# Kernel tuning notes

Measured on AMD Instinct MI355X. Metric: run time of the kernel, lower is better.

The kernel has to match this reference:

```python
import jax, jax.numpy as jnp
import numpy as np

B, A, N_IN, N_POINTS = 64, 256, 512, 2048


def _sq_cdist(u, v):
    # |u_i - v_j|^2 via expansion, abs() as in the torch original
    d = -2.0 * (u @ v.T) + (u * u).sum(1)[:, None] + (v * v).sum(1)[None, :]
    return jnp.abs(d)


def setup_inputs() -> dict:
    key = jax.random.key(0)
    k1, k2, k3, k4 = jax.random.split(key, 4)
    x = jax.random.normal(k1, (B, A, N_IN), dtype=jnp.float32)
    atom_mask = jax.random.bernoulli(k2, 0.8, (B, A))  # ragged valid-atom mask
    inducing_points = jax.random.normal(k3, (N_POINTS, N_IN), dtype=jnp.float32)
    gamma = (1.0 + 0.25 * jax.random.normal(k4, (N_IN,), dtype=jnp.float32)) * np.sqrt(N_IN).astype(np.float32)
    return {"x": x, "atom_mask": atom_mask, "inducing_points": inducing_points, "gamma": gamma}


def reference(x, atom_mask, inducing_points, gamma):
    b, a, n_in = x.shape
    m = atom_mask.astype(x.dtype)                      # [B, A]
    mf = m[..., None]                                  # [B, A, 1]
    n = m.sum()
    # masked mean / unbiased std over valid atoms (torch .std is ddof=1)
    mean = (x * mf).sum((0, 1)) / n                    # [n_in]
    var = (((x - mean) ** 2) * mf).sum((0, 1)) / (n - 1.0)
    std = jnp.sqrt(var) + 1e-5                         # [n_in]
    xn = (x - mean) / std * mf                         # zero out padded atoms

    g2 = gamma ** 2 + 0.001                            # [n_in]
    z = (xn / g2).reshape(b * a, n_in)                 # [N, n_in]
    zi = inducing_points / g2                          # [M, n_in]

    Kx = jnp.exp(-_sq_cdist(z, zi))                    # [N, M]
    Kind = jnp.exp(-_sq_cdist(zi, zi))                 # [M, M]
    Kinv = jnp.linalg.inv(Kind + 0.05 * jnp.eye(Kind.shape[0], dtype=x.dtype))

    t = Kx @ Kinv                                      # [N, M]
    x_new = ((t @ inducing_points) * std + mean).reshape(b, a, n_in) * mf
    var_out = (1.0 - (t * Kx).sum(-1)).reshape(b, a) * m
    return x_new, var_out
```

## Files before the change

### kernel.cpp

```cpp
#include <hip/hip_runtime.h>
#include <math.h>
#include <stdint.h>

namespace {

constexpr int NROW = 16384;
constexpr int NF   = 512;
constexpr int MIND = 2048;
constexpr float CC = 0.98f;

typedef _Float16 half8 __attribute__((ext_vector_type(8)));
typedef float floatx4 __attribute__((ext_vector_type(4)));

__device__ __forceinline__ void gload16(const void* g, void* l) {
  __builtin_amdgcn_global_load_lds(
      (__attribute__((address_space(1))) void*)g,
      (__attribute__((address_space(3))) void*)l, 16, 0, 0);
}

#define MEMFENCE asm volatile("" ::: "memory")
#define GATE(N) asm volatile("s_waitcnt vmcnt(" #N ")" ::: "memory")

__global__ __launch_bounds__(256) void stats_kernel(
    const float* __restrict__ x, const int* __restrict__ mask,
    float* __restrict__ sum, float* __restrict__ sumsq, float* __restrict__ cnt)
{
  const int t = threadIdx.x;
  const int row0 = blockIdx.x * 64;
  float s0 = 0.f, s1 = 0.f, q0 = 0.f, q1 = 0.f, c = 0.f;
  for (int r = 0; r < 64; ++r) {
    const int row = row0 + r;
    const float m = (mask[row] != 0) ? 1.f : 0.f;
    const float v0 = x[(size_t)row * NF + t];
    const float v1 = x[(size_t)row * NF + t + 256];
    s0 += m * v0; q0 += m * v0 * v0;
    s1 += m * v1; q1 += m * v1 * v1;
    c += m;
  }
  atomicAdd(&sum[t], s0);        atomicAdd(&sum[t + 256], s1);
  atomicAdd(&sumsq[t], q0);      atomicAdd(&sumsq[t + 256], q1);
  if (t == 0) atomicAdd(cnt, c);
}

__global__ __launch_bounds__(256) void finalize_stats(
    const float* __restrict__ sum, const float* __restrict__ sumsq,
    const float* __restrict__ cnt, const float* __restrict__ gamma,
    float* __restrict__ meanv, float* __restrict__ stdv,
    float* __restrict__ zsv, float* __restrict__ giv)
{
  const int f = blockIdx.x * 256 + threadIdx.x;
  const float n = cnt[0];
  const float mu = sum[f] / n;
  const float var = (sumsq[f] - sum[f] * mu) / (n - 1.0f);
  const float sd = sqrtf(var) + 1e-5f;
  const float g = gamma[f];
  const float g2 = g * g + 0.001f;
  meanv[f] = mu;
  stdv[f]  = sd;
  zsv[f]   = 1.0f / (sd * g2);
  giv[f]   = 1.0f / g2;
}

__global__ __launch_bounds__(256) void make_z(
    const float* __restrict__ x, const int* __restrict__ mask,
    const float* __restrict__ ip, const float* __restrict__ meanv,
    const float* __restrict__ zsv, const float* __restrict__ giv,
    _Float16* __restrict__ Zh, _Float16* __restrict__ Zih,
    float* __restrict__ rnorm, float* __restrict__ cnorm)
{
  const int row = blockIdx.x;
  const int t = threadIdx.x;
  float v0, v1;
  if (row < NROW) {
    const float m = (mask[row] != 0) ? 1.f : 0.f;
    v0 = (x[(size_t)row * NF + t      ] - meanv[t      ]) * zsv[t      ] * m;
    v1 = (x[(size_t)row * NF + t + 256] - meanv[t + 256]) * zsv[t + 256] * m;
    const _Float16 h0 = (_Float16)v0, h1 = (_Float16)v1;
    Zh[(size_t)row * NF + t] = h0;
    Zh[(size_t)row * NF + t + 256] = h1;
    v0 = (float)h0; v1 = (float)h1;
  } else {
    const int r = row - NROW;
    v0 = ip[(size_t)r * NF + t      ] * giv[t      ];
    v1 = ip[(size_t)r * NF + t + 256] * giv[t + 256];
    const _Float16 h0 = (_Float16)v0, h1 = (_Float16)v1;
    Zih[(size_t)r * NF + t] = h0;
    Zih[(size_t)r * NF + t + 256] = h1;
    v0 = (float)h0; v1 = (float)h1;
  }
  float nrm = v0 * v0 + v1 * v1;
  #pragma unroll
  for (int off = 32; off; off >>= 1) nrm += __shfl_xor(nrm, off);
  __shared__ float red[4];
  if ((t & 63) == 0) red[t >> 6] = nrm;
  __syncthreads();
  if (t == 0) {
    const float s = red[0] + red[1] + red[2] + red[3];
    if (row < NROW) rnorm[row] = s; else cnorm[row - NROW] = s;
  }
}

template <int EPI>
__global__ __launch_bounds__(512, 2) void mfma_gemm256(
    const _Float16* __restrict__ A, const _Float16* __restrict__ B,
    int M, int N, int K,
    const float* __restrict__ rn, const float* __restrict__ cn,
    _Float16* __restrict__ DKout,
    const _Float16* __restrict__ DK, const float* __restrict__ u,
    float* __restrict__ varacc)
{
  __shared__ __align__(16) _Float16 Asmem[4][256 * 32];
  __shared__ __align__(16) _Float16 Bsmem[4][256 * 32];

  const int tid = threadIdx.x;
  const int w = tid >> 6, L = tid & 63;
  const int wm = w >> 2, wn = w & 3;
  const int lq = L >> 4, lr = L & 15;
  const int bn = blockIdx.x, bm = blockIdx.y;
  const int NT = K >> 5;

  const int srow  = tid >> 2;
  const int sslot = tid & 3;
  const int gslot = sslot ^ ((tid >> 3) & 3);
  const _Float16* Ag = A + (size_t)(bm * 256 + srow) * K + gslot * 8;
  const _Float16* Bg = B + (size_t)(bn * 256 + srow) * K + gslot * 8;
  const size_t rstride = (size_t)128 * K;
  const int ldst = srow * 32 + sslot * 8;

  const int fswz = (lq ^ ((lr >> 1) & 3)) * 8;
  const int aoff = (wm * 128 + lr) * 32 + fswz;
  const int boff = (wn * 64  + lr) * 32 + fswz;

  floatx4 acc[8][4] = {};

  auto stageA = [&](int t) {
    _Float16* dst = Asmem[t & 3] + ldst;
    const _Float16* src = Ag + (size_t)t * 32;
    gload16(src, dst);
    gload16(src + rstride, dst + 128 * 32);
  };
  auto stageB = [&](int t) {
    _Float16* dst = Bsmem[t & 3] + ldst;
    const _Float16* src = Bg + (size_t)t * 32;
    gload16(src, dst);
    gload16(src + rstride, dst + 128 * 32);
  };

  stageA(0); stageB(0);
  if (NT > 1) { stageA(1); stageB(1); }
  if (NT > 2) { stageA(2); stageB(2); }
  if (NT > 2)      { GATE(8); }
  else if (NT > 1) { GATE(4); }
  else             { GATE(0); }
  __builtin_amdgcn_s_barrier();
  MEMFENCE;

  for (int t = 0; t < NT; ++t) {
    const _Float16* As = Asmem[t & 3];
    const _Float16* Bs = Bsmem[t & 3];
    half8 af[4], bf[4], af2[4];

    #pragma unroll
    for (int mi = 0; mi < 4; ++mi) af[mi] = *(const half8*)&As[aoff + mi * 512];
    #pragma unroll
    for (int ni = 0; ni < 4; ++ni) bf[ni] = *(const half8*)&Bs[boff + ni * 512];
    if (t + 3 < NT) stageA(t + 3);
    MEMFENCE;
    __builtin_amdgcn_s_barrier();
    MEMFENCE;
    __builtin_amdgcn_s_setprio(1);
    #pragma unroll
    for (int mi = 0; mi < 4; ++mi)
      #pragma unroll
      for (int ni = 0; ni < 4; ++ni)
        acc[mi][ni] = __builtin_amdgcn_mfma_f32_16x16x32_f16(
            af[mi], bf[ni], acc[mi][ni], 0, 0, 0);
    __builtin_amdgcn_s_setprio(0);

    #pragma unroll
    for (int mi = 0; mi < 4; ++mi)
      af2[mi] = *(const half8*)&As[aoff + (mi + 4) * 512];
    if (t + 3 < NT) stageB(t + 3);
    if (t + 4 <= NT)      { GATE(8); }
    else if (t + 3 == NT) { GATE(4); }
    else if (t + 2 == NT) { GATE(0); }
    __builtin_amdgcn_s_barrier();
    MEMFENCE;
    __builtin_amdgcn_s_setprio(1);
    #pragma unroll
    for (int mi = 0; mi < 4; ++mi)
      #pragma unroll
      for (int ni = 0; ni < 4; ++ni)
        acc[mi + 4][ni] = __builtin_amdgcn_mfma_f32_16x16x32_f16(
            af2[mi], bf[ni], acc[mi + 4][ni], 0, 0, 0);
    __builtin_amdgcn_s_setprio(0);
  }

  const int grb = bm * 256 + wm * 128;
  const int gcb = bn * 256 + wn * 64;

  if constexpr (EPI == 0) {
    #pragma unroll
    for (int mi = 0; mi < 8; ++mi)
      #pragma unroll
      for (int e = 0; e < 4; ++e) {
        const int gr = grb + mi * 16 + lq * 4 + e;
        const float rni = rn[gr];
        #pragma unroll
        for (int ni = 0; ni < 4; ++ni) {
          const int gc = gcb + ni * 16 + lr;
          const float d = rni + cn[gc] - 2.f * acc[mi][ni][e];
          DKout[(size_t)gr * N + gc] = (_Float16)(expf(-fabsf(d)) - CC);
        }
      }
  } else {
    #pragma unroll
    for (int mi = 0; mi < 8; ++mi)
      #pragma unroll
      for (int e = 0; e < 4; ++e) {
        const int gr = grb + mi * 16 + lq * 4 + e;
        float partial = 0.f;
        #pragma unroll
        for (int ni = 0; ni < 4; ++ni) {
          const int gc = gcb + ni * 16 + lr;
          const float tv = acc[mi][ni][e] + CC * u[gc];
          partial += tv * (CC + (float)DK[(size_t)gr * N + gc]);
        }
        partial += __shfl_xor(partial, 1);
        partial += __shfl_xor(partial, 2);
        partial += __shfl_xor(partial, 4);
        partial += __shfl_xor(partial, 8);
        if (lr == 0) atomicAdd(&varacc[gr], partial);
      }
  }
}

template <int EPI>
__global__ __launch_bounds__(256) void mfma_gemm(
    const _Float16* __restrict__ A, const _Float16* __restrict__ B,
    int M, int N, int K,
    const float* __restrict__ rn, const float* __restrict__ cn,
    _Float16* __restrict__ DKout, float* __restrict__ Cf,
    const _Float16* __restrict__ DK, const float* __restrict__ u,
    float* __restrict__ varacc,
    const float* __restrict__ colsumR,
    const float* __restrict__ stdv, const float* __restrict__ meanv,
    const int* __restrict__ mask)
{
  __shared__ __align__(16) _Float16 As[128 * 32];
  __shared__ __align__(16) _Float16 Bs[128 * 32];
  const int tid = threadIdx.x;
  const int w = tid >> 6, L = tid & 63;
  const int wm = w >> 1, wn = w & 1;
  const int bn = blockIdx.x, bm = blockIdx.y;
  const int lq = L >> 4;
  const int lr = L & 15;

  floatx4 acc[4][4] = {};

  const _Float16* Ag = A + (size_t)(bm * 128) * K;
  const _Float16* Bg = B + (size_t)(bn * 128) * K;
  const int srow = w * 32 + (L >> 2);
  const int scol = (L & 3) * 8;

  for (int k0 = 0; k0 < K; k0 += 32) {
    #pragma unroll
    for (int t = 0; t < 2; ++t) {
      const int r = srow + t * 16;
      gload16(Ag + (size_t)r * K + k0 + scol, As + r * 32 + scol);
      gload16(Bg + (size_t)r * K + k0 + scol, Bs + r * 32 + scol);
    }
    __syncthreads();
    half8 af[4], bf[4];
    #pragma unroll
    for (int mi = 0; mi < 4; ++mi)
      af[mi] = *(const half8*)&As[(wm * 64 + mi * 16 + lr) * 32 + lq * 8];
    #pragma unroll
    for (int ni = 0; ni < 4; ++ni)
      bf[ni] = *(const half8*)&Bs[(wn * 64 + ni * 16 + lr) * 32 + lq * 8];
    #pragma unroll
    for (int mi = 0; mi < 4; ++mi)
      #pragma unroll
      for (int ni = 0; ni < 4; ++ni)
        acc[mi][ni] = __builtin_amdgcn_mfma_f32_16x16x32_f16(
            af[mi], bf[ni], acc[mi][ni], 0, 0, 0);
    __syncthreads();
  }

  const int grb = bm * 128 + wm * 64;
  const int gcb = bn * 128 + wn * 64;

  if constexpr (EPI == 3) {
    #pragma unroll
    for (int mi = 0; mi < 4; ++mi)
      #pragma unroll
      for (int e = 0; e < 4; ++e) {
        const int gr = grb + mi * 16 + lq * 4 + e;
        const float mrow = (mask[gr] != 0) ? 1.f : 0.f;
        #pragma unroll
        for (int ni = 0; ni < 4; ++ni) {
          const int gc = gcb + ni * 16 + lr;
          const float v = acc[mi][ni][e] + CC * colsumR[gc];
          Cf[(size_t)gr * N + gc] = (v * stdv[gc] + meanv[gc]) * mrow;
        }
      }
  } else {
    #pragma unroll
    for (int mi = 0; mi < 4; ++mi)
      #pragma unroll
      for (int e = 0; e < 4; ++e) {
        const int gr = grb + mi * 16 + lq * 4 + e;
        const float rni = rn[gr];
        #pragma unroll
        for (int ni = 0; ni < 4; ++ni) {
          const int gc = gcb + ni * 16 + lr;
          const float d = rni + cn[gc] - 2.f * acc[mi][ni][e];
          float kx = expf(-fabsf(d));
          if (gr == gc) kx += 0.05f;
          Cf[(size_t)gr * N + gc] = kx;
        }
      }
  }
}

__global__ __launch_bounds__(256) void gemm_f32(
    const float* __restrict__ A, const float* __restrict__ B,
    float* __restrict__ C, int M, int N, int K)
{
  constexpr int BM = 64, BN = 64, BK = 16;
  const int tid = threadIdx.x;
  const int tx = tid % 16, ty = tid / 16;
  const int bn = blockIdx.x, bm = blockIdx.y;
  __shared__ float As[BK][BM + 4];
  __shared__ float Bs[BK][BN + 4];
  float acc[4][4] = {};
  const float* Ag = A + (size_t)bm * BM * K;
  const float* Bg = B + bn * BN;
  for (int k0 = 0; k0 < K; k0 += BK) {
    {
      const int r = tid >> 2, c4 = (tid & 3) << 2;
      const float4 av = *(const float4*)(Ag + (size_t)r * K + k0 + c4);
      As[c4 + 0][r] = av.x; As[c4 + 1][r] = av.y;
      As[c4 + 2][r] = av.z; As[c4 + 3][r] = av.w;
      const int kr = tid / 16, nc = (tid % 16) << 2;
      *(float4*)&Bs[kr][nc] = *(const float4*)(Bg + (size_t)(k0 + kr) * N + nc);
    }
    __syncthreads();
    #pragma unroll
    for (int kk = 0; kk < BK; ++kk) {
      const float4 a4 = *(const float4*)&As[kk][ty * 4];
      const float4 b4 = *(const float4*)&Bs[kk][tx * 4];
      const float a[4] = {a4.x, a4.y, a4.z, a4.w};
      const float b[4] = {b4.x, b4.y, b4.z, b4.w};
      #pragma unroll
      for (int i = 0; i < 4; ++i)
        #pragma unroll
        for (int j = 0; j < 4; ++j) acc[i][j] += a[i] * b[j];
    }
    __syncthreads();
  }
  #pragma unroll
  for (int i = 0; i < 4; ++i) {
    float4 o4; o4.x = acc[i][0]; o4.y = acc[i][1]; o4.z = acc[i][2]; o4.w = acc[i][3];
    *(float4*)(C + (size_t)(bm * BM + ty * 4 + i) * N + bn * BN + tx * 4) = o4;
  }
}


__global__ __launch_bounds__(256) void gj_diag(
    float* __restrict__ A, float* __restrict__ Pall, int k)
{
  const int o = k * 64;
  __shared__ float D[64][68];
  const int t = threadIdx.x;
  #pragma unroll
  for (int l = 0; l < 4; ++l) {
    const int v = t + l * 256;
    const int r = v >> 4, c4 = (v & 15) << 2;
    *(float4*)&D[r][c4] = *(const float4*)(A + (size_t)(o + r) * MIND + o + c4);
  }
  __syncthreads();
  const int i = t >> 2, c0 = (t & 3) * 16;
  for (int s = 0; s < 64; ++s) {
    const float p = 1.0f / D[s][s];
    if (t < 64 && t != s) D[s][t] *= p;
    __syncthreads();
    if (i != s) {
      const float f = D[i][s];
      #pragma unroll
      for (int c = c0; c < c0 + 16; c += 4) {
        float4 ds = *(const float4*)&D[s][c];
        float4 di = *(const float4*)&D[i][c];
        di.x -= f * ds.x; di.y -= f * ds.y; di.z -= f * ds.z; di.w -= f * ds.w;
        *(float4*)&D[i][c] = di;
      }
      if (s >= c0 && s < c0 + 16) D[i][s] = -f * p;
    }
    if (t == 0) D[s][s] = p;
    __syncthreads();
  }
  float* P = Pall + k * 4096;
  #pragma unroll
  for (int l = 0; l < 4; ++l) {
    const int v = t + l * 256;
    const int r = v >> 4, c4 = (v & 15) << 2;
    const float4 dv = *(const float4*)&D[r][c4];
    *(float4*)(P + r * 64 + c4) = dv;
    *(float4*)(A + (size_t)(o + r) * MIND + o + c4) = dv;
  }
}

__global__ __launch_bounds__(256) void gj_prep(
    const float* __restrict__ A, const float* __restrict__ Pall,
    float* __restrict__ CP, float* __restrict__ Bsave, int k)
{
  const int o = k * 64;
  const int t = threadIdx.x;
  if (blockIdx.x >= 32) {
    const int j0 = (blockIdx.x - 32) * 64;
    #pragma unroll
    for (int l = 0; l < 4; ++l) {
      const int v = t + l * 256;
      const int r = v >> 4, c4 = (v & 15) << 2;
      *(float4*)(Bsave + r * MIND + j0 + c4) =
          *(const float4*)(A + (size_t)(o + r) * MIND + j0 + c4);
    }
    return;
  }
  const int i0 = blockIdx.x * 64;
  if (i0 == o) return;
  const float* P = Pall + k * 4096;
  __shared__ float At[64][68];
  __shared__ float Pl[64][68];
  #pragma unroll
  for (int l = 0; l < 4; ++l) {
    const int v = t + l * 256;
    const int r = v >> 4, c4 = (v & 15) << 2;
    const float4 av = *(const float4*)(A + (size_t)(i0 + r) * MIND + o + c4);
    At[c4 + 0][r] = av.x; At[c4 + 1][r] = av.y;
    At[c4 + 2][r] = av.z; At[c4 + 3][r] = av.w;
    *(float4*)&Pl[r][c4] = *(const float4*)(P + r * 64 + c4);
  }
  __syncthreads();
  const int ty = t >> 4, tx = t & 15;
  float acc[4][4] = {};
  for (int s = 0; s < 64; ++s) {
    const float4 a4 = *(const float4*)&At[s][ty * 4];
    const float4 b4 = *(const float4*)&Pl[s][tx * 4];
    const float a[4] = {a4.x, a4.y, a4.z, a4.w};
    const float b[4] = {b4.x, b4.y, b4.z, b4.w};
    #pragma unroll
    for (int i = 0; i < 4; ++i)
      #pragma unroll
      for (int j = 0; j < 4; ++j) acc[i][j] += a[i] * b[j];
  }
  #pragma unroll
  for (int i = 0; i < 4; ++i) {
    float4 o4; o4.x = acc[i][0]; o4.y = acc[i][1]; o4.z = acc[i][2]; o4.w = acc[i][3];
    *(float4*)(CP + (i0 + ty * 4 + i) * 64 + tx * 4) = o4;
  }
}

__global__ __launch_bounds__(256) void gj_apply(
    float* __restrict__ A, float* __restrict__ Pall,
    const float* __restrict__ CP, const float* __restrict__ Bsave, int k)
{
  const int o = k * 64;
  const int i0 = blockIdx.y * 64, j0 = blockIdx.x * 64;
  const int t = threadIdx.x;

  if (i0 == o && j0 == o) return;

  if (j0 == o) {
    #pragma unroll
    for (int l = 0; l < 4; ++l) {
      const int v = t + l * 256;
      const int r = v >> 4, c4 = (v & 15) << 2;
      float4 x = *(const float4*)(CP + (i0 + r) * 64 + c4);
      x.x = -x.x; x.y = -x.y; x.z = -x.z; x.w = -x.w;
      *(float4*)(A + (size_t)(i0 + r) * MIND + o + c4) = x;
    }
    return;
  }

  __shared__ float S1[64 * 68];
  __shared__ float S2[64 * 68];
  #define DD(r, c) S1[(r) * 68 + (c)]

  const bool isrow = (i0 == o);
  const float* Lsrc = isrow ? (Pall + k * 4096) : (CP + i0 * 64);
  #pragma unroll
  for (int l = 0; l < 4; ++l) {
    const int v = t + l * 256;
    const int r = v >> 4, c4 = (v & 15) << 2;
    const float4 lv = *(const float4*)(Lsrc + r * 64 + c4);
    S1[(c4 + 0) * 68 + r] = lv.x; S1[(c4 + 1) * 68 + r] = lv.y;
    S1[(c4 + 2) * 68 + r] = lv.z; S1[(c4 + 3) * 68 + r] = lv.w;
    *(float4*)&S2[r * 68 + c4] = *(const float4*)(Bsave + r * MIND + j0 + c4);
  }
  __syncthreads();
  const int ty = t >> 4, tx = t & 15;
  float acc[4][4] = {};
  for (int s = 0; s < 64; ++s) {
    const float4 a4 = *(const float4*)&S1[s * 68 + ty * 4];
    const float4 b4 = *(const float4*)&S2[s * 68 + tx * 4];
    const float a[4] = {a4.x, a4.y, a4.z, a4.w};
    const float b[4] = {b4.x, b4.y, b4.z, b4.w};
    #pragma unroll
    for (int i = 0; i < 4; ++i)
      #pragma unroll
      for (int j = 0; j < 4; ++j) acc[i][j] += a[i] * b[j];
  }

  if (isrow) {
    #pragma unroll
    for (int i = 0; i < 4; ++i) {
      float4 o4; o4.x = acc[i][0]; o4.y = acc[i][1]; o4.z = acc[i][2]; o4.w = acc[i][3];
      *(float4*)(A + (size_t)(o + ty * 4 + i) * MIND + j0 + tx * 4) = o4;
    }
    return;
  }

  const bool isdiagnext = (i0 == o + 64) && (j0 == o + 64);
  if (!isdiagnext) {
    #pragma unroll
    for (int i = 0; i < 4; ++i) {
      float* cp = A + (size_t)(i0 + ty * 4 + i) * MIND + j0 + tx * 4;
      float4 cv = *(const float4*)cp;
      cv.x -= acc[i][0]; cv.y -= acc[i][1]; cv.z -= acc[i][2]; cv.w -= acc[i][3];
      *(float4*)cp = cv;
    }
    return;
  }

  __syncthreads();
  #pragma unroll
  for (int i = 0; i < 4; ++i) {
    const float4 cv = *(const float4*)(A + (size_t)(i0 + ty * 4 + i) * MIND + j0 + tx * 4);
    DD(ty * 4 + i, tx * 4 + 0) = cv.x - acc[i][0];
    DD(ty * 4 + i, tx * 4 + 1) = cv.y - acc[i][1];
    DD(ty * 4 + i, tx * 4 + 2) = cv.z - acc[i][2];
    DD(ty * 4 + i, tx * 4 + 3) = cv.w - acc[i][3];
  }
  __syncthreads();
  const int di = t >> 2, c0 = (t & 3) * 16;
  for (int s = 0; s < 64; ++s) {
    const float p = 1.0f / DD(s, s);
    if (t < 64 && t != s) DD(s, t) *= p;
    __syncthreads();
    if (di != s) {
      const float f = DD(di, s);
      #pragma unroll
      for (int c = c0; c < c0 + 16; c += 4) {
        float4 ds = *(const float4*)&DD(s, c);
        float4 dv = *(const float4*)&DD(di, c);
        dv.x -= f * ds.x; dv.y -= f * ds.y; dv.z -= f * ds.z; dv.w -= f * ds.w;
        *(float4*)&DD(di, c) = dv;
      }
      if (s >= c0 && s < c0 + 16) DD(di, s) = -f * p;
    }
    if (t == 0) DD(s, s) = p;
    __syncthreads();
  }
  float* Pn = Pall + (k + 1) * 4096;
  #pragma unroll
  for (int l = 0; l < 4; ++l) {
    const int v = t + l * 256;
    const int r = v >> 4, c4 = (v & 15) << 2;
    const float4 dv = *(const float4*)&DD(r, c4);
    *(float4*)(Pn + r * 64 + c4) = dv;
    *(float4*)(A + (size_t)(i0 + r) * MIND + j0 + c4) = dv;
  }
  #undef DD
}

__global__ __launch_bounds__(256) void rowsum_kernel(
    const float* __restrict__ Ai, float* __restrict__ u)
{
  const int row = blockIdx.x * 4 + (threadIdx.x >> 6);
  const int lane = threadIdx.x & 63;
  float s = 0.f;
  for (int c = lane; c < MIND; c += 64) s += Ai[(size_t)row * MIND + c];
  #pragma unroll
  for (int off = 32; off; off >>= 1) s += __shfl_xor(s, off);
  if (lane == 0) u[row] = s;
}

typedef _Float16 half4v __attribute__((ext_vector_type(4)));
__global__ __launch_bounds__(256) void cast_half4(
    const float* __restrict__ s, _Float16* __restrict__ d)
{
  const int i = (blockIdx.x * 256 + threadIdx.x) * 4;
  const float4 v = *(const float4*)(s + i);
  half4v h; h.x = (_Float16)v.x; h.y = (_Float16)v.y;
  h.z = (_Float16)v.z; h.w = (_Float16)v.w;
  *(half4v*)(d + i) = h;
}

__global__ __launch_bounds__(256) void transpose_cast(
    const float* __restrict__ R, _Float16* __restrict__ Rt)
{
  __shared__ float T[64][65];
  const int j0 = blockIdx.x * 64;
  const int f0 = blockIdx.y * 64;
  const int t = threadIdx.x;
  #pragma unroll
  for (int l = 0; l < 16; ++l) {
    const int idx = t + l * 256;
    T[idx >> 6][idx & 63] = R[(size_t)(j0 + (idx >> 6)) * NF + f0 + (idx & 63)];
  }
  __syncthreads();
  #pragma unroll
  for (int l = 0; l < 16; ++l) {
    const int idx = t + l * 256;
    const int fr = idx >> 6, jc = idx & 63;
    Rt[(size_t)(f0 + fr) * MIND + j0 + jc] = (_Float16)T[jc][fr];
  }
}

__global__ __launch_bounds__(256) void colsum_kernel(
    const float* __restrict__ R, float* __restrict__ cs)
{
  const int b = blockIdx.x;
  const int t = threadIdx.x;
  float s0 = 0.f, s1 = 0.f;
  for (int r = 0; r < 64; ++r) {
    s0 += R[(size_t)(b * 64 + r) * NF + t];
    s1 += R[(size_t)(b * 64 + r) * NF + t + 256];
  }
  atomicAdd(&cs[t], s0); atomicAdd(&cs[t + 256], s1);
}

__global__ __launch_bounds__(256) void var_finalize(
    const float* __restrict__ varacc, const int* __restrict__ mask,
    float* __restrict__ outv)
{
  const int i = blockIdx.x * 256 + threadIdx.x;
  const float m = (mask[i] != 0) ? 1.f : 0.f;
  outv[i] = (1.0f - varacc[i]) * m;
}

}

extern "C" void kernel_launch(void* const* d_in, const int* in_sizes, int n_in,
                              void* d_out, int out_size, void* d_ws, size_t ws_size,
                              hipStream_t stream)
{
  (void)in_sizes; (void)n_in; (void)out_size; (void)ws_size;
  const float* x     = (const float*)d_in[0];
  const int*   mask  = (const int*)d_in[1];
  const float* ip    = (const float*)d_in[2];
  const float* gamma = (const float*)d_in[3];
  float* out = (float*)d_out;

  float* w       = (float*)d_ws;
  float* sum     = w;
  float* sumsq   = w + 512;
  float* cnt     = w + 1024;
  float* varacc  = w + 1536;
  float* colsumR = w + 17920;
  float* meanv   = w + 18432;
  float* stdv    = w + 18944;
  float* zsv     = w + 19456;
  float* giv     = w + 19968;
  float* rnorm   = w + 20480;
  float* cnorm   = w + 36864;
  float* u       = w + 38912;
  float* Ai      = w + 40960;
  float* R       = w + 4235264;
  float* Pall    = w + 5283840;
  float* CP      = w + 5414912;
  float* Bsave   = w + 5545984;
  _Float16* hb   = (_Float16*)(w + 5677056);
  _Float16* Zh   = hb;
  _Float16* Zih  = hb + 8388608;
  _Float16* DK   = hb + 9437184;
  _Float16* Kih  = hb + 42991616;
  _Float16* Rt   = hb + 47185920;

  hipMemsetAsync(w, 0, 18432 * sizeof(float), stream);

  stats_kernel<<<256, 256, 0, stream>>>(x, mask, sum, sumsq, cnt);
  finalize_stats<<<2, 256, 0, stream>>>(sum, sumsq, cnt, gamma, meanv, stdv, zsv, giv);
  make_z<<<NROW + MIND, 256, 0, stream>>>(x, mask, ip, meanv, zsv, giv, Zh, Zih, rnorm, cnorm);

  mfma_gemm256<0><<<dim3(MIND / 256, NROW / 256), 512, 0, stream>>>(
      Zh, Zih, NROW, MIND, NF, rnorm, cnorm,
      DK, nullptr, nullptr, nullptr);
  mfma_gemm<1><<<dim3(MIND / 128, MIND / 128), 256, 0, stream>>>(
      Zih, Zih, MIND, MIND, NF, cnorm, cnorm,
      nullptr, Ai, nullptr, nullptr, nullptr, nullptr, nullptr, nullptr, nullptr);

  gj_diag<<<1, 256, 0, stream>>>(Ai, Pall, 0);
  gj_prep<<<64, 256, 0, stream>>>(Ai, Pall, CP, Bsave, 0);
  for (int k = 0; k < 32; ++k) {
    gj_apply<<<dim3(32, 32), 256, 0, stream>>>(Ai, Pall, CP, Bsave, k);
    if (k < 31) gj_prep<<<64, 256, 0, stream>>>(Ai, Pall, CP, Bsave, k + 1);
  }

  gemm_f32<<<dim3(NF / 64, MIND / 64), 256, 0, stream>>>(Ai, ip, R, MIND, NF, MIND);
  transpose_cast<<<dim3(MIND / 64, NF / 64), 256, 0, stream>>>(R, Rt);
  colsum_kernel<<<MIND / 64, 256, 0, stream>>>(R, colsumR);
  rowsum_kernel<<<MIND / 4, 256, 0, stream>>>(Ai, u);
  cast_half4<<<(MIND * MIND) / 1024, 256, 0, stream>>>(Ai, Kih);

  mfma_gemm256<2><<<dim3(MIND / 256, NROW / 256), 512, 0, stream>>>(
      DK, Kih, NROW, MIND, MIND, nullptr, nullptr,
      nullptr, DK, u, varacc);

  mfma_gemm<3><<<dim3(NF / 128, NROW / 128), 256, 0, stream>>>(
      DK, Rt, NROW, NF, MIND, nullptr, nullptr,
      nullptr, out, nullptr, nullptr, nullptr, colsumR, stdv, meanv, mask);

  var_finalize<<<NROW / 256, 256, 0, stream>>>(varacc, mask, out + (size_t)NROW * NF);
}
```

Measured before the change: 2.110 ms.

## Fuse Gauss-Jordan prep into apply kernel and double-buffer MFMA fragment loads

The block Gauss-Jordan inversion no longer launches a separate prep kernel per step. Each apply block recomputes its CP panel product locally and writes the next step's pivot row and column panels into ping-pong buffers, which halves the number of launches across the 32 steps. The 256-tile MFMA GEMM main loop is unrolled by two with register double buffering, so the next tile's A/B fragments are read from LDS during the current tile's second MFMA half. The cost is redundant panel GEMMs in every apply block and higher register pressure in the GEMM.

Result: slower. 2.173 ms (+3.0%).

```diff
diff --git a/kernel.cpp b/kernel.cpp
--- a/kernel.cpp
+++ b/kernel.cpp
@@ -155,15 +155,24 @@
   __builtin_amdgcn_s_barrier();
   MEMFENCE;
 
-  for (int t = 0; t < NT; ++t) {
+  half8 afA[4], bfA[4], afB[4], bfB[4];
+  {
+    const _Float16* As0 = Asmem[0];
+    const _Float16* Bs0 = Bsmem[0];
+    #pragma unroll
+    for (int mi = 0; mi < 4; ++mi) afA[mi] = *(const half8*)&As0[aoff + mi * 512];
+    #pragma unroll
+    for (int ni = 0; ni < 4; ++ni) bfA[ni] = *(const half8*)&Bs0[boff + ni * 512];
+  }
+
+  auto tile_body = [&](int t, half8 (&ac)[4], half8 (&bc)[4],
+                       half8 (&an)[4], half8 (&bnx)[4]) {
     const _Float16* As = Asmem[t & 3];
-    const _Float16* Bs = Bsmem[t & 3];
-    half8 af[4], bf[4], af2[4];
-
-    #pragma unroll
-    for (int mi = 0; mi < 4; ++mi) af[mi] = *(const half8*)&As[aoff + mi * 512];
-    #pragma unroll
-    for (int ni = 0; ni < 4; ++ni) bf[ni] = *(const half8*)&Bs[boff + ni * 512];
+    half8 af2[4];
+
+    #pragma unroll
+    for (int mi = 0; mi < 4; ++mi)
+      af2[mi] = *(const half8*)&As[aoff + (mi + 4) * 512];
     if (t + 3 < NT) stageA(t + 3);
     MEMFENCE;
     __builtin_amdgcn_s_barrier();
@@ -174,26 +183,38 @@
       #pragma unroll
       for (int ni = 0; ni < 4; ++ni)
         acc[mi][ni] = __builtin_amdgcn_mfma_f32_16x16x32_f16(
-            af[mi], bf[ni], acc[mi][ni], 0, 0, 0);
+            ac[mi], bc[ni], acc[mi][ni], 0, 0, 0);
     __builtin_amdgcn_s_setprio(0);
 
-    #pragma unroll
-    for (int mi = 0; mi < 4; ++mi)
-      af2[mi] = *(const half8*)&As[aoff + (mi + 4) * 512];
     if (t + 3 < NT) stageB(t + 3);
     if (t + 4 <= NT)      { GATE(8); }
     else if (t + 3 == NT) { GATE(4); }
     else if (t + 2 == NT) { GATE(0); }
     __builtin_amdgcn_s_barrier();
     MEMFENCE;
+    if (t + 1 < NT) {
+      const _Float16* As1 = Asmem[(t + 1) & 3];
+      const _Float16* Bs1 = Bsmem[(t + 1) & 3];
+      #pragma unroll
+      for (int mi = 0; mi < 4; ++mi)
+        an[mi] = *(const half8*)&As1[aoff + mi * 512];
+      #pragma unroll
+      for (int ni = 0; ni < 4; ++ni)
+        bnx[ni] = *(const half8*)&Bs1[boff + ni * 512];
+    }
     __builtin_amdgcn_s_setprio(1);
     #pragma unroll
     for (int mi = 0; mi < 4; ++mi)
       #pragma unroll
       for (int ni = 0; ni < 4; ++ni)
         acc[mi + 4][ni] = __builtin_amdgcn_mfma_f32_16x16x32_f16(
-            af2[mi], bf[ni], acc[mi + 4][ni], 0, 0, 0);
+            af2[mi], bc[ni], acc[mi + 4][ni], 0, 0, 0);
     __builtin_amdgcn_s_setprio(0);
+  };
+
+  for (int t = 0; t < NT; t += 2) {
+    tile_body(t,     afA, bfA, afB, bfB);
+    tile_body(t + 1, afB, bfB, afA, bfA);
   }
 
   const int grb = bm * 256 + wm * 128;
@@ -367,17 +388,42 @@
 }
 
 
-__global__ __launch_bounds__(256) void gj_diag(
-    float* __restrict__ A, float* __restrict__ Pall, int k)
-{
-  const int o = k * 64;
+__global__ __launch_bounds__(256) void gj_diag2(
+    float* __restrict__ A, float* __restrict__ Pall,
+    float* __restrict__ CPr, float* __restrict__ Bsv)
+{
+  const int t = threadIdx.x;
+  const int b = blockIdx.x;
+  if (b > 0) {
+    if (b <= 32) {
+      if (b == 1) return;
+      const int r0 = (b - 1) * 64;
+      #pragma unroll
+      for (int l = 0; l < 4; ++l) {
+        const int v = t + l * 256;
+        const int r = v >> 4, c4 = (v & 15) << 2;
+        *(float4*)(CPr + (r0 + r) * 64 + c4) =
+            *(const float4*)(A + (size_t)(r0 + r) * MIND + c4);
+      }
+    } else {
+      if (b == 33) return;
+      const int j0 = (b - 33) * 64;
+      #pragma unroll
+      for (int l = 0; l < 4; ++l) {
+        const int v = t + l * 256;
+        const int r = v >> 4, c4 = (v & 15) << 2;
+        *(float4*)(Bsv + r * MIND + j0 + c4) =
+            *(const float4*)(A + (size_t)r * MIND + j0 + c4);
+      }
+    }
+    return;
+  }
   __shared__ float D[64][68];
-  const int t = threadIdx.x;
   #pragma unroll
   for (int l = 0; l < 4; ++l) {
     const int v = t + l * 256;
     const int r = v >> 4, c4 = (v & 15) << 2;
-    *(float4*)&D[r][c4] = *(const float4*)(A + (size_t)(o + r) * MIND + o + c4);
+    *(float4*)&D[r][c4] = *(const float4*)(A + (size_t)r * MIND + c4);
   }
   __syncthreads();
   const int i = t >> 2, c0 = (t & 3) * 16;
@@ -399,107 +445,110 @@
     if (t == 0) D[s][s] = p;
     __syncthreads();
   }
-  float* P = Pall + k * 4096;
   #pragma unroll
   for (int l = 0; l < 4; ++l) {
     const int v = t + l * 256;
     const int r = v >> 4, c4 = (v & 15) << 2;
     const float4 dv = *(const float4*)&D[r][c4];
-    *(float4*)(P + r * 64 + c4) = dv;
-    *(float4*)(A + (size_t)(o + r) * MIND + o + c4) = dv;
-  }
-}
-
-__global__ __launch_bounds__(256) void gj_prep(
-    const float* __restrict__ A, const float* __restrict__ Pall,
-    float* __restrict__ CP, float* __restrict__ Bsave, int k)
+    *(float4*)(Pall + r * 64 + c4) = dv;
+    *(float4*)(A + (size_t)r * MIND + c4) = dv;
+  }
+}
+
+__global__ __launch_bounds__(256) void gj_apply2(
+    float* __restrict__ A, float* __restrict__ Pall,
+    const float* __restrict__ CPr, const float* __restrict__ Bsv,
+    float* __restrict__ CPrN, float* __restrict__ BsvN, int k)
 {
   const int o = k * 64;
+  const int i0 = blockIdx.y * 64, j0 = blockIdx.x * 64;
   const int t = threadIdx.x;
-  if (blockIdx.x >= 32) {
-    const int j0 = (blockIdx.x - 32) * 64;
+  if (i0 == o && j0 == o) return;
+
+  __shared__ float S1[64 * 68];
+  __shared__ float S2[64 * 68];
+  #define DD(r, c) S1[(r) * 68 + (c)]
+  const int ty = t >> 4, tx = t & 15;
+  const float* P = Pall + (size_t)k * 4096;
+  const bool iNext = (i0 == o + 64);
+  const bool jNext = (j0 == o + 64);
+
+  if (i0 == o) {
     #pragma unroll
     for (int l = 0; l < 4; ++l) {
       const int v = t + l * 256;
       const int r = v >> 4, c4 = (v & 15) << 2;
-      *(float4*)(Bsave + r * MIND + j0 + c4) =
-          *(const float4*)(A + (size_t)(o + r) * MIND + j0 + c4);
+      const float4 lv = *(const float4*)(P + r * 64 + c4);
+      S1[(c4 + 0) * 68 + r] = lv.x; S1[(c4 + 1) * 68 + r] = lv.y;
+      S1[(c4 + 2) * 68 + r] = lv.z; S1[(c4 + 3) * 68 + r] = lv.w;
+      *(float4*)&S2[r * 68 + c4] = *(const float4*)(Bsv + r * MIND + j0 + c4);
+    }
+    __syncthreads();
+    float acc[4][4] = {};
+    for (int s = 0; s < 64; ++s) {
+      const float4 a4 = *(const float4*)&S1[s * 68 + ty * 4];
+      const float4 b4 = *(const float4*)&S2[s * 68 + tx * 4];
+      const float a[4] = {a4.x, a4.y, a4.z, a4.w};
+      const float b[4] = {b4.x, b4.y, b4.z, b4.w};
+      #pragma unroll
+      for (int i = 0; i < 4; ++i)
+        #pragma unroll
+        for (int j = 0; j < 4; ++j) acc[i][j] += a[i] * b[j];
+    }
+    #pragma unroll
+    for (int i = 0; i < 4; ++i) {
+      float4 o4; o4.x = acc[i][0]; o4.y = acc[i][1]; o4.z = acc[i][2]; o4.w = acc[i][3];
+      *(float4*)(A + (size_t)(o + ty * 4 + i) * MIND + j0 + tx * 4) = o4;
+      if (jNext) *(float4*)(CPrN + (o + ty * 4 + i) * 64 + tx * 4) = o4;
     }
     return;
   }
-  const int i0 = blockIdx.x * 64;
-  if (i0 == o) return;
-  const float* P = Pall + k * 4096;
-  __shared__ float At[64][68];
-  __shared__ float Pl[64][68];
+
   #pragma unroll
   for (int l = 0; l < 4; ++l) {
     const int v = t + l * 256;
     const int r = v >> 4, c4 = (v & 15) << 2;
-    const float4 av = *(const float4*)(A + (size_t)(i0 + r) * MIND + o + c4);
-    At[c4 + 0][r] = av.x; At[c4 + 1][r] = av.y;
-    At[c4 + 2][r] = av.z; At[c4 + 3][r] = av.w;
-    *(float4*)&Pl[r][c4] = *(const float4*)(P + r * 64 + c4);
+    const float4 av = *(const float4*)(CPr + (i0 + r) * 64 + c4);
+    S1[(c4 + 0) * 68 + r] = av.x; S1[(c4 + 1) * 68 + r] = av.y;
+    S1[(c4 + 2) * 68 + r] = av.z; S1[(c4 + 3) * 68 + r] = av.w;
+    *(float4*)&S2[r * 68 + c4] = *(const float4*)(P + r * 64 + c4);
   }
   __syncthreads();
-  const int ty = t >> 4, tx = t & 15;
-  float acc[4][4] = {};
+  float cp[4][4] = {};
   for (int s = 0; s < 64; ++s) {
-    const float4 a4 = *(const float4*)&At[s][ty * 4];
-    const float4 b4 = *(const float4*)&Pl[s][tx * 4];
+    const float4 a4 = *(const float4*)&S1[s * 68 + ty * 4];
+    const float4 b4 = *(const float4*)&S2[s * 68 + tx * 4];
     const float a[4] = {a4.x, a4.y, a4.z, a4.w};
     const float b[4] = {b4.x, b4.y, b4.z, b4.w};
     #pragma unroll
     for (int i = 0; i < 4; ++i)
       #pragma unroll
-      for (int j = 0; j < 4; ++j) acc[i][j] += a[i] * b[j];
-  }
-  #pragma unroll
-  for (int i = 0; i < 4; ++i) {
-    float4 o4; o4.x = acc[i][0]; o4.y = acc[i][1]; o4.z = acc[i][2]; o4.w = acc[i][3];
-    *(float4*)(CP + (i0 + ty * 4 + i) * 64 + tx * 4) = o4;
-  }
-}
-
-__global__ __launch_bounds__(256) void gj_apply(
-    float* __restrict__ A, float* __restrict__ Pall,
-    const float* __restrict__ CP, const float* __restrict__ Bsave, int k)
-{
-  const int o = k * 64;
-  const int i0 = blockIdx.y * 64, j0 = blockIdx.x * 64;
-  const int t = threadIdx.x;
-
-  if (i0 == o && j0 == o) return;
+      for (int j = 0; j < 4; ++j) cp[i][j] += a[i] * b[j];
+  }
 
   if (j0 == o) {
     #pragma unroll
-    for (int l = 0; l < 4; ++l) {
-      const int v = t + l * 256;
-      const int r = v >> 4, c4 = (v & 15) << 2;
-      float4 x = *(const float4*)(CP + (i0 + r) * 64 + c4);
-      x.x = -x.x; x.y = -x.y; x.z = -x.z; x.w = -x.w;
-      *(float4*)(A + (size_t)(i0 + r) * MIND + o + c4) = x;
+    for (int i = 0; i < 4; ++i) {
+      float4 o4; o4.x = -cp[i][0]; o4.y = -cp[i][1]; o4.z = -cp[i][2]; o4.w = -cp[i][3];
+      *(float4*)(A + (size_t)(i0 + ty * 4 + i) * MIND + o + tx * 4) = o4;
+      if (iNext) *(float4*)(BsvN + (ty * 4 + i) * MIND + o + tx * 4) = o4;
     }
     return;
   }
 
-  __shared__ float S1[64 * 68];
-  __shared__ float S2[64 * 68];
-  #define DD(r, c) S1[(r) * 68 + (c)]
-
-  const bool isrow = (i0 == o);
-  const float* Lsrc = isrow ? (Pall + k * 4096) : (CP + i0 * 64);
+  __syncthreads();
+  #pragma unroll
+  for (int i = 0; i < 4; ++i)
+    #pragma unroll
+    for (int j = 0; j < 4; ++j)
+      S1[(tx * 4 + j) * 68 + (ty * 4 + i)] = cp[i][j];
   #pragma unroll
   for (int l = 0; l < 4; ++l) {
     const int v = t + l * 256;
     const int r = v >> 4, c4 = (v & 15) << 2;
-    const float4 lv = *(const float4*)(Lsrc + r * 64 + c4);
-    S1[(c4 + 0) * 68 + r] = lv.x; S1[(c4 + 1) * 68 + r] = lv.y;
-    S1[(c4 + 2) * 68 + r] = lv.z; S1[(c4 + 3) * 68 + r] = lv.w;
-    *(float4*)&S2[r * 68 + c4] = *(const float4*)(Bsave + r * MIND + j0 + c4);
+    *(float4*)&S2[r * 68 + c4] = *(const float4*)(Bsv + r * MIND + j0 + c4);
   }
   __syncthreads();
-  const int ty = t >> 4, tx = t & 15;
   float acc[4][4] = {};
   for (int s = 0; s < 64; ++s) {
     const float4 a4 = *(const float4*)&S1[s * 68 + ty * 4];
@@ -512,23 +561,16 @@
       for (int j = 0; j < 4; ++j) acc[i][j] += a[i] * b[j];
   }
 
-  if (isrow) {
+  const bool isdiagnext = iNext && jNext;
+  if (!isdiagnext) {
     #pragma unroll
     for (int i = 0; i < 4; ++i) {
-      float4 o4; o4.x = acc[i][0]; o4.y = acc[i][1]; o4.z = acc[i][2]; o4.w = acc[i][3];
-      *(float4*)(A + (size_t)(o + ty * 4 + i) * MIND + j0 + tx * 4) = o4;
-    }
-    return;
-  }
-
-  const bool isdiagnext = (i0 == o + 64) && (j0 == o + 64);
-  if (!isdiagnext) {
-    #pragma unroll
-    for (int i = 0; i < 4; ++i) {
-      float* cp = A + (size_t)(i0 + ty * 4 + i) * MIND + j0 + tx * 4;
-      float4 cv = *(const float4*)cp;
+      float* cpp = A + (size_t)(i0 + ty * 4 + i) * MIND + j0 + tx * 4;
+      float4 cv = *(const float4*)cpp;
       cv.x -= acc[i][0]; cv.y -= acc[i][1]; cv.z -= acc[i][2]; cv.w -= acc[i][3];
-      *(float4*)cp = cv;
+      *(float4*)cpp = cv;
+      if (iNext) *(float4*)(BsvN + (ty * 4 + i) * MIND + j0 + tx * 4) = cv;
+      if (jNext) *(float4*)(CPrN + (i0 + ty * 4 + i) * 64 + tx * 4) = cv;
     }
     return;
   }
@@ -562,7 +604,7 @@
     if (t == 0) DD(s, s) = p;
     __syncthreads();
   }
-  float* Pn = Pall + (k + 1) * 4096;
+  float* Pn = Pall + (size_t)(k + 1) * 4096;
   #pragma unroll
   for (int l = 0; l < 4; ++l) {
     const int v = t + l * 256;
@@ -668,6 +710,8 @@
   float* u       = w + 38912;
   float* Ai      = w + 40960;
   float* R       = w + 4235264;
+  float* CP2     = w + 4235264;
+  float* Bs2     = w + 4366336;
   float* Pall    = w + 5283840;
   float* CP      = w + 5414912;
   float* Bsave   = w + 5545984;
@@ -691,11 +735,13 @@
       Zih, Zih, MIND, MIND, NF, cnorm, cnorm,
       nullptr, Ai, nullptr, nullptr, nullptr, nullptr, nullptr, nullptr, nullptr);
 
-  gj_diag<<<1, 256, 0, stream>>>(Ai, Pall, 0);
-  gj_prep<<<64, 256, 0, stream>>>(Ai, Pall, CP, Bsave, 0);
+  gj_diag2<<<65, 256, 0, stream>>>(Ai, Pall, CP, Bsave);
   for (int k = 0; k < 32; ++k) {
-    gj_apply<<<dim3(32, 32), 256, 0, stream>>>(Ai, Pall, CP, Bsave, k);
-    if (k < 31) gj_prep<<<64, 256, 0, stream>>>(Ai, Pall, CP, Bsave, k + 1);
+    const bool e = (k & 1) == 0;
+    gj_apply2<<<dim3(32, 32), 256, 0, stream>>>(
+        Ai, Pall,
+        e ? CP : CP2, e ? Bsave : Bs2,
+        e ? CP2 : CP, e ? Bs2 : Bsave, k);
   }
 
   gemm_f32<<<dim3(NF / 64, MIND / 64), 256, 0, stream>>>(Ai, ip, R, MIND, NF, MIND);
```

## Merge GEMM launches into pipelined 256-tile kernel via concatenated operands

Applied to the files above, without the earlier changes.

The Kx and Kind distance GEMMs become a single launch of the pipelined 256-tile MFMA kernel. This relies on Zih following Zh in memory and cnorm following rnorm, and each block picks its epilogue from its tile index. The t·Kx variance GEMM and the output GEMM against Rt are also merged into one launch by treating Kih and Rt as one stacked B matrix. Separately, transpose+colsum and rowsum+cast are each fused into one kernel. The aim is to drop the slow unpipelined 128-tile GEMM and several launches and extra passes over Ai and R. The risk is that correctness now depends on the exact workspace layout.

Result: no change. 2.123 ms (+0.6%).

```diff
diff --git a/kernel.cpp b/kernel.cpp
--- a/kernel.cpp
+++ b/kernel.cpp
@@ -10,6 +10,7 @@
 constexpr float CC = 0.98f;
 
 typedef _Float16 half8 __attribute__((ext_vector_type(8)));
+typedef _Float16 half4v __attribute__((ext_vector_type(4)));
 typedef float floatx4 __attribute__((ext_vector_type(4)));
 
 __device__ __forceinline__ void gload16(const void* g, void* l) {
@@ -100,14 +101,15 @@
   }
 }
 
-template <int EPI>
-__global__ __launch_bounds__(512, 2) void mfma_gemm256(
-    const _Float16* __restrict__ A, const _Float16* __restrict__ B,
-    int M, int N, int K,
+template <int PASS>
+__global__ __launch_bounds__(512, 2) void mfma_gemm256f(
+    const _Float16* __restrict__ A, const _Float16* __restrict__ B, int K,
     const float* __restrict__ rn, const float* __restrict__ cn,
-    _Float16* __restrict__ DKout,
+    _Float16* __restrict__ DKout, float* __restrict__ Cf,
     const _Float16* __restrict__ DK, const float* __restrict__ u,
-    float* __restrict__ varacc)
+    float* __restrict__ varacc,
+    const float* __restrict__ colsumR, const float* __restrict__ stdv,
+    const float* __restrict__ meanv, const int* __restrict__ mask)
 {
   __shared__ __align__(16) _Float16 Asmem[4][256 * 32];
   __shared__ __align__(16) _Float16 Bsmem[4][256 * 32];
@@ -199,127 +201,75 @@
   const int grb = bm * 256 + wm * 128;
   const int gcb = bn * 256 + wn * 64;
 
-  if constexpr (EPI == 0) {
-    #pragma unroll
-    for (int mi = 0; mi < 8; ++mi)
-      #pragma unroll
-      for (int e = 0; e < 4; ++e) {
-        const int gr = grb + mi * 16 + lq * 4 + e;
-        const float rni = rn[gr];
+  if constexpr (PASS == 0) {
+    if (bm < NROW / 256) {
+      #pragma unroll
+      for (int mi = 0; mi < 8; ++mi)
         #pragma unroll
-        for (int ni = 0; ni < 4; ++ni) {
-          const int gc = gcb + ni * 16 + lr;
-          const float d = rni + cn[gc] - 2.f * acc[mi][ni][e];
-          DKout[(size_t)gr * N + gc] = (_Float16)(expf(-fabsf(d)) - CC);
+        for (int e = 0; e < 4; ++e) {
+          const int gr = grb + mi * 16 + lq * 4 + e;
+          const float rni = rn[gr];
+          #pragma unroll
+          for (int ni = 0; ni < 4; ++ni) {
+            const int gc = gcb + ni * 16 + lr;
+            const float d = rni + cn[gc] - 2.f * acc[mi][ni][e];
+            DKout[(size_t)gr * MIND + gc] = (_Float16)(expf(-fabsf(d)) - CC);
+          }
         }
-      }
+    } else {
+      #pragma unroll
+      for (int mi = 0; mi < 8; ++mi)
+        #pragma unroll
+        for (int e = 0; e < 4; ++e) {
+          const int gr = grb + mi * 16 + lq * 4 + e;
+          const int gr2 = gr - NROW;
+          const float rni = rn[gr];
+          #pragma unroll
+          for (int ni = 0; ni < 4; ++ni) {
+            const int gc = gcb + ni * 16 + lr;
+            const float d = rni + cn[gc] - 2.f * acc[mi][ni][e];
+            float kx = expf(-fabsf(d));
+            if (gr2 == gc) kx += 0.05f;
+            Cf[(size_t)gr2 * MIND + gc] = kx;
+          }
+        }
+    }
   } else {
-    #pragma unroll
-    for (int mi = 0; mi < 8; ++mi)
-      #pragma unroll
-      for (int e = 0; e < 4; ++e) {
-        const int gr = grb + mi * 16 + lq * 4 + e;
-        float partial = 0.f;
+    if (bn < MIND / 256) {
+      #pragma unroll
+      for (int mi = 0; mi < 8; ++mi)
         #pragma unroll
-        for (int ni = 0; ni < 4; ++ni) {
-          const int gc = gcb + ni * 16 + lr;
-          const float tv = acc[mi][ni][e] + CC * u[gc];
-          partial += tv * (CC + (float)DK[(size_t)gr * N + gc]);
+        for (int e = 0; e < 4; ++e) {
+          const int gr = grb + mi * 16 + lq * 4 + e;
+          float partial = 0.f;
+          #pragma unroll
+          for (int ni = 0; ni < 4; ++ni) {
+            const int gc = gcb + ni * 16 + lr;
+            const float tv = acc[mi][ni][e] + CC * u[gc];
+            partial += tv * (CC + (float)DK[(size_t)gr * MIND + gc]);
+          }
+          partial += __shfl_xor(partial, 1);
+          partial += __shfl_xor(partial, 2);
+          partial += __shfl_xor(partial, 4);
+          partial += __shfl_xor(partial, 8);
+          if (lr == 0) atomicAdd(&varacc[gr], partial);
         }
-        partial += __shfl_xor(partial, 1);
-        partial += __shfl_xor(partial, 2);
-        partial += __shfl_xor(partial, 4);
-        partial += __shfl_xor(partial, 8);
-        if (lr == 0) atomicAdd(&varacc[gr], partial);
-      }
-  }
-}
-
-template <int EPI>
-__global__ __launch_bounds__(256) void mfma_gemm(
-    const _Float16* __restrict__ A, const _Float16* __restrict__ B,
-    int M, int N, int K,
-    const float* __restrict__ rn, const float* __restrict__ cn,
-    _Float16* __restrict__ DKout, float* __restrict__ Cf,
-    const _Float16* __restrict__ DK, const float* __restrict__ u,
-    float* __restrict__ varacc,
-    const float* __restrict__ colsumR,
-    const float* __restrict__ stdv, const float* __restrict__ meanv,
-    const int* __restrict__ mask)
-{
-  __shared__ __align__(16) _Float16 As[128 * 32];
-  __shared__ __align__(16) _Float16 Bs[128 * 32];
-  const int tid = threadIdx.x;
-  const int w = tid >> 6, L = tid & 63;
-  const int wm = w >> 1, wn = w & 1;
-  const int bn = blockIdx.x, bm = blockIdx.y;
-  const int lq = L >> 4;
-  const int lr = L & 15;
-
-  floatx4 acc[4][4] = {};
-
-  const _Float16* Ag = A + (size_t)(bm * 128) * K;
-  const _Float16* Bg = B + (size_t)(bn * 128) * K;
-  const int srow = w * 32 + (L >> 2);
-  const int scol = (L & 3) * 8;
-
-  for (int k0 = 0; k0 < K; k0 += 32) {
-    #pragma unroll
-    for (int t = 0; t < 2; ++t) {
-      const int r = srow + t * 16;
-      gload16(Ag + (size_t)r * K + k0 + scol, As + r * 32 + scol);
-      gload16(Bg + (size_t)r * K + k0 + scol, Bs + r * 32 + scol);
-    }
-    __syncthreads();
-    half8 af[4], bf[4];
-    #pragma unroll
-    for (int mi = 0; mi < 4; ++mi)
-      af[mi] = *(const half8*)&As[(wm * 64 + mi * 16 + lr) * 32 + lq * 8];
-    #pragma unroll
-    for (int ni = 0; ni < 4; ++ni)
-      bf[ni] = *(const half8*)&Bs[(wn * 64 + ni * 16 + lr) * 32 + lq * 8];
-    #pragma unroll
-    for (int mi = 0; mi < 4; ++mi)
-      #pragma unroll
-      for (int ni = 0; ni < 4; ++ni)
-        acc[mi][ni] = __builtin_amdgcn_mfma_f32_16x16x32_f16(
-            af[mi], bf[ni], acc[mi][ni], 0, 0, 0);
-    __syncthreads();
-  }
-
-  const int grb = bm * 128 + wm * 64;
-  const int gcb = bn * 128 + wn * 64;
-
-  if constexpr (EPI == 3) {
-    #pragma unroll
-    for (int mi = 0; mi < 4; ++mi)
-      #pragma unroll
-      for (int e = 0; e < 4; ++e) {
-        const int gr = grb + mi * 16 + lq * 4 + e;
-        const float mrow = (mask[gr] != 0) ? 1.f : 0.f;
+    } else {
+      const int gcb3 = (bn - MIND / 256) * 256 + wn * 64;
+      #pragma unroll
+      for (int mi = 0; mi < 8; ++mi)
         #pragma unroll
-        for (int ni = 0; ni < 4; ++ni) {
-          const int gc = gcb + ni * 16 + lr;
-          const float v = acc[mi][ni][e] + CC * colsumR[gc];
-          Cf[(size_t)gr * N + gc] = (v * stdv[gc] + meanv[gc]) * mrow;
+        for (int e = 0; e < 4; ++e) {
+          const int gr = grb + mi * 16 + lq * 4 + e;
+          const float mrow = (mask[gr] != 0) ? 1.f : 0.f;
+          #pragma unroll
+          for (int ni = 0; ni < 4; ++ni) {
+            const int gc3 = gcb3 + ni * 16 + lr;
+            const float v = acc[mi][ni][e] + CC * colsumR[gc3];
+            Cf[(size_t)gr * NF + gc3] = (v * stdv[gc3] + meanv[gc3]) * mrow;
+          }
         }
-      }
-  } else {
-    #pragma unroll
-    for (int mi = 0; mi < 4; ++mi)
-      #pragma unroll
-      for (int e = 0; e < 4; ++e) {
-        const int gr = grb + mi * 16 + lq * 4 + e;
-        const float rni = rn[gr];
-        #pragma unroll
-        for (int ni = 0; ni < 4; ++ni) {
-          const int gc = gcb + ni * 16 + lr;
-          const float d = rni + cn[gc] - 2.f * acc[mi][ni][e];
-          float kx = expf(-fabsf(d));
-          if (gr == gc) kx += 0.05f;
-          Cf[(size_t)gr * N + gc] = kx;
-        }
-      }
+    }
   }
 }
 
@@ -574,33 +524,35 @@
   #undef DD
 }
 
-__global__ __launch_bounds__(256) void rowsum_kernel(
-    const float* __restrict__ Ai, float* __restrict__ u)
+__global__ __launch_bounds__(256) void rowsum_cast(
+    const float* __restrict__ Ai, float* __restrict__ u,
+    _Float16* __restrict__ Kih)
 {
   const int row = blockIdx.x * 4 + (threadIdx.x >> 6);
   const int lane = threadIdx.x & 63;
+  const float* src = Ai + (size_t)row * MIND;
+  _Float16* dst = Kih + (size_t)row * MIND;
   float s = 0.f;
-  for (int c = lane; c < MIND; c += 64) s += Ai[(size_t)row * MIND + c];
+  #pragma unroll
+  for (int it = 0; it < 8; ++it) {
+    const int c = it * 256 + lane * 4;
+    const float4 v = *(const float4*)(src + c);
+    s += v.x + v.y + v.z + v.w;
+    half4v h; h.x = (_Float16)v.x; h.y = (_Float16)v.y;
+    h.z = (_Float16)v.z; h.w = (_Float16)v.w;
+    *(half4v*)(dst + c) = h;
+  }
   #pragma unroll
   for (int off = 32; off; off >>= 1) s += __shfl_xor(s, off);
   if (lane == 0) u[row] = s;
 }
 
-typedef _Float16 half4v __attribute__((ext_vector_type(4)));
-__global__ __launch_bounds__(256) void cast_half4(
-    const float* __restrict__ s, _Float16* __restrict__ d)
-{
-  const int i = (blockIdx.x * 256 + threadIdx.x) * 4;
-  const float4 v = *(const float4*)(s + i);
-  half4v h; h.x = (_Float16)v.x; h.y = (_Float16)v.y;
-  h.z = (_Float16)v.z; h.w = (_Float16)v.w;
-  *(half4v*)(d + i) = h;
-}
-
-__global__ __launch_bounds__(256) void transpose_cast(
-    const float* __restrict__ R, _Float16* __restrict__ Rt)
+__global__ __launch_bounds__(256) void transpose_colsum(
+    const float* __restrict__ R, _Float16* __restrict__ Rt,
+    float* __restrict__ cs)
 {
   __shared__ float T[64][65];
+  __shared__ float psum[4][64];
   const int j0 = blockIdx.x * 64;
   const int f0 = blockIdx.y * 64;
   const int t = threadIdx.x;
@@ -616,19 +568,13 @@
     const int fr = idx >> 6, jc = idx & 63;
     Rt[(size_t)(f0 + fr) * MIND + j0 + jc] = (_Float16)T[jc][fr];
   }
-}
-
-__global__ __launch_bounds__(256) void colsum_kernel(
-    const float* __restrict__ R, float* __restrict__ cs)
-{
-  const int b = blockIdx.x;
-  const int t = threadIdx.x;
-  float s0 = 0.f, s1 = 0.f;
-  for (int r = 0; r < 64; ++r) {
-    s0 += R[(size_t)(b * 64 + r) * NF + t];
-    s1 += R[(size_t)(b * 64 + r) * NF + t + 256];
-  }
-  atomicAdd(&cs[t], s0); atomicAdd(&cs[t + 256], s1);
+  const int f = t & 63, q = t >> 6;
+  float s = 0.f;
+  #pragma unroll
+  for (int j = q * 16; j < q * 16 + 16; ++j) s += T[j][f];
+  psum[q][f] = s;
+  __syncthreads();
+  if (t < 64) atomicAdd(&cs[f0 + t], psum[0][t] + psum[1][t] + psum[2][t] + psum[3][t]);
 }
 
 __global__ __launch_bounds__(256) void var_finalize(
@@ -684,12 +630,9 @@
   finalize_stats<<<2, 256, 0, stream>>>(sum, sumsq, cnt, gamma, meanv, stdv, zsv, giv);
   make_z<<<NROW + MIND, 256, 0, stream>>>(x, mask, ip, meanv, zsv, giv, Zh, Zih, rnorm, cnorm);
 
-  mfma_gemm256<0><<<dim3(MIND / 256, NROW / 256), 512, 0, stream>>>(
-      Zh, Zih, NROW, MIND, NF, rnorm, cnorm,
-      DK, nullptr, nullptr, nullptr);
-  mfma_gemm<1><<<dim3(MIND / 128, MIND / 128), 256, 0, stream>>>(
-      Zih, Zih, MIND, MIND, NF, cnorm, cnorm,
-      nullptr, Ai, nullptr, nullptr, nullptr, nullptr, nullptr, nullptr, nullptr);
+  mfma_gemm256f<0><<<dim3(MIND / 256, (NROW + MIND) / 256), 512, 0, stream>>>(
+      Zh, Zih, NF, rnorm, cnorm,
+      DK, Ai, nullptr, nullptr, nullptr, nullptr, nullptr, nullptr, nullptr);
 
   gj_diag<<<1, 256, 0, stream>>>(Ai, Pall, 0);
   gj_prep<<<64, 256, 0, stream>>>(Ai, Pall, CP, Bsave, 0);
@@ -699,18 +642,12 @@
   }
 
   gemm_f32<<<dim3(NF / 64, MIND / 64), 256, 0, stream>>>(Ai, ip, R, MIND, NF, MIND);
-  transpose_cast<<<dim3(MIND / 64, NF / 64), 256, 0, stream>>>(R, Rt);
-  colsum_kernel<<<MIND / 64, 256, 0, stream>>>(R, colsumR);
-  rowsum_kernel<<<MIND / 4, 256, 0, stream>>>(Ai, u);
-  cast_half4<<<(MIND * MIND) / 1024, 256, 0, stream>>>(Ai, Kih);
-
-  mfma_gemm256<2><<<dim3(MIND / 256, NROW / 256), 512, 0, stream>>>(
-      DK, Kih, NROW, MIND, MIND, nullptr, nullptr,
-      nullptr, DK, u, varacc);
-
-  mfma_gemm<3><<<dim3(NF / 128, NROW / 128), 256, 0, stream>>>(
-      DK, Rt, NROW, NF, MIND, nullptr, nullptr,
-      nullptr, out, nullptr, nullptr, nullptr, colsumR, stdv, meanv, mask);
+  transpose_colsum<<<dim3(MIND / 64, NF / 64), 256, 0, stream>>>(R, Rt, colsumR);
+  rowsum_cast<<<MIND / 4, 256, 0, stream>>>(Ai, u, Kih);
+
+  mfma_gemm256f<1><<<dim3((MIND + NF) / 256, NROW / 256), 512, 0, stream>>>(
+      DK, Kih, MIND, nullptr, nullptr,
+      nullptr, out, DK, u, varacc, colsumR, stdv, meanv, mask);
 
   var_finalize<<<NROW / 256, 256, 0, stream>>>(varacc, mask, out + (size_t)NROW * NF);
 }
```
